# Kernel optimization log

Hardware: AMD Instinct MI355X
Metric: run time of the kernel (lower is better)

The kernel has to match this reference:

```python
import jax, jax.numpy as jnp
import numpy as np


def setup_inputs() -> dict:
    key = jax.random.key(0)
    k1, k2 = jax.random.split(key)
    x = jax.random.normal(k1, (4, 2048, 2048), dtype=jnp.float32)
    weight = jax.random.normal(k2, (8192, 2048), dtype=jnp.float32) * 0.02
    return {"x": x, "weight": weight, "bits": 8}


def reference(x, weight, bits):
    # ---- activation quantization (per-row int8-style) ----
    scale = jnp.clip(jnp.max(jnp.abs(x), axis=-1, keepdims=True), 1e-5)  # [..., 1]
    max_val = (1 << (bits - 1)) - 1  # 127 for 8 bits
    x_q = jnp.clip(jnp.round(x * (max_val / scale)), -max_val, max_val)

    # ---- ternary weight quantization (-1, 0, 1) ----
    w_scale = jnp.mean(jnp.abs(weight))
    w_q = jnp.where(weight > 0.5 * w_scale, 1.0, 0.0) + jnp.where(
        weight < -0.5 * w_scale, -1.0, 0.0
    )

    # ---- dequantized linear: (x_q @ (w_q * w_scale)^T) / x_scale ----
    out = jnp.einsum("bsi,oi->bso", x_q, w_q * w_scale) / scale

    # ---- squared ReLU ----
    return jnp.maximum(out, 0.0) ** 2
```

## Files before the change

kernel.cpp:

```cpp
#include <hip/hip_runtime.h>
#include <hip/hip_bf16.h>

typedef __attribute__((ext_vector_type(4))) int i32x4;
typedef __attribute__((ext_vector_type(16))) int i32x16;

#define M_DIM 8192
#define N_DIM 8192
#define K_DIM 2048
#define WCOUNT (N_DIM * K_DIM)

__global__ __launch_bounds__(256) void k_abs_partial(const float* __restrict__ w,
                                                     float* __restrict__ part) {
    int tid = blockIdx.x * 256 + threadIdx.x;
    const float4* w4 = (const float4*)w;
    float s = 0.0f;
    const int total4 = WCOUNT / 4;
    for (int i = tid; i < total4; i += 2048 * 256) {
        float4 v = w4[i];
        s += fabsf(v.x) + fabsf(v.y) + fabsf(v.z) + fabsf(v.w);
    }
    #pragma unroll
    for (int off = 1; off < 64; off <<= 1) s += __shfl_xor(s, off);
    __shared__ float red[4];
    if ((threadIdx.x & 63) == 0) red[threadIdx.x >> 6] = s;
    __syncthreads();
    if (threadIdx.x == 0)
        part[blockIdx.x] = (red[0] + red[1]) + (red[2] + red[3]);
}

__global__ __launch_bounds__(256) void k_abs_final(const float* __restrict__ part,
                                                   float* __restrict__ sum) {
    int t = threadIdx.x;
    float s = 0.0f;
    #pragma unroll
    for (int i = 0; i < 8; i++) s += part[t + i * 256];
    #pragma unroll
    for (int off = 1; off < 64; off <<= 1) s += __shfl_xor(s, off);
    __shared__ float red[4];
    if ((t & 63) == 0) red[t >> 6] = s;
    __syncthreads();
    if (t == 0) sum[0] = (red[0] + red[1]) + (red[2] + red[3]);
}

__global__ __launch_bounds__(256) void k_wquant(const float* __restrict__ w,
                                                const float* __restrict__ sum,
                                                unsigned int* __restrict__ wq) {
    const float thr = 0.5f * (sum[0] * (1.0f / 16777216.0f));
    int tid = blockIdx.x * 256 + threadIdx.x;
    const float4* w4 = (const float4*)w;
    const int total4 = WCOUNT / 4;
    for (int i = tid; i < total4; i += 2048 * 256) {
        float4 v = w4[i];
        union { signed char c[4]; unsigned int u; } q;
        q.c[0] = v.x > thr ? 1 : (v.x < -thr ? -1 : 0);
        q.c[1] = v.y > thr ? 1 : (v.y < -thr ? -1 : 0);
        q.c[2] = v.z > thr ? 1 : (v.z < -thr ? -1 : 0);
        q.c[3] = v.w > thr ? 1 : (v.w < -thr ? -1 : 0);
        wq[i] = q.u;
    }
}

__global__ __launch_bounds__(256) void k_xquant(const float* __restrict__ x,
                                                signed char* __restrict__ xq,
                                                float* __restrict__ scale) {
    const int row = blockIdx.x;
    const int t = threadIdx.x;
    const float4* xr = (const float4*)(x + (size_t)row * K_DIM);
    float4 a = xr[t * 2];
    float4 b = xr[t * 2 + 1];
    float m = fmaxf(fmaxf(fmaxf(fabsf(a.x), fabsf(a.y)), fmaxf(fabsf(a.z), fabsf(a.w))),
                    fmaxf(fmaxf(fabsf(b.x), fabsf(b.y)), fmaxf(fabsf(b.z), fabsf(b.w))));
    #pragma unroll
    for (int off = 1; off < 64; off <<= 1) m = fmaxf(m, __shfl_xor(m, off));
    __shared__ float red[4];
    if ((t & 63) == 0) red[t >> 6] = m;
    __syncthreads();
    m = fmaxf(fmaxf(red[0], red[1]), fmaxf(red[2], red[3]));
    const float sc = fmaxf(m, 1e-5f);
    if (t == 0) scale[row] = sc;
    const float r = 127.0f / sc;
    float q[8] = {a.x, a.y, a.z, a.w, b.x, b.y, b.z, b.w};
    union { signed char c[8]; uint2 v; } pk;
    #pragma unroll
    for (int j = 0; j < 8; j++) {
        float v = rintf(q[j] * r);
        v = fminf(fmaxf(v, -127.0f), 127.0f);
        pk.c[j] = (signed char)v;
    }
    *(uint2*)(xq + (size_t)row * K_DIM + t * 8) = pk.v;
}

__global__ __launch_bounds__(256) void k_coef(const float* __restrict__ sum,
                                              const float* __restrict__ scale,
                                              float* __restrict__ coef) {
    const int i = blockIdx.x * 256 + threadIdx.x;
    coef[i] = (sum[0] * (1.0f / 16777216.0f)) / scale[i];
}

#define GLDS16(g, l)                                                                   \
    __builtin_amdgcn_global_load_lds((const __attribute__((address_space(1))) void*)(g), \
                                     (__attribute__((address_space(3))) void*)(l), 16, 0, 0)

#define BAR __builtin_amdgcn_s_barrier()
#define VMCNT3 asm volatile("s_waitcnt vmcnt(3)" ::: "memory")
#define VMCNT0 asm volatile("s_waitcnt vmcnt(0)" ::: "memory")
#define ABUF(b) ((b) * 24576)
#define BBUF(b) ((b) * 24576 + 8192)

__global__ __launch_bounds__(512, 4) void k_gemm(const signed char* __restrict__ Aq,
                                                 const signed char* __restrict__ Bq,
                                                 const float* __restrict__ coef,
                                                 float* __restrict__ out) {
    __shared__ signed char lds[49152];

    const int t = threadIdx.x;
    const int lane = t & 63;
    const int wid = t >> 6;
    const int wm = wid >> 2;
    const int wn = wid & 3;
    const int l31 = lane & 31;
    const int kg = lane >> 5;

    const int bid = blockIdx.x;
    const int xcd = bid & 7;
    const int idx = bid >> 3;
    const int bcol = (idx >> 5) * 4 + (idx & 3);
    const int brow = xcd * 8 + ((idx >> 2) & 7);

    const int g4 = ((t & 3) ^ ((t >> 3) & 3)) << 4;
    const int arow_s = t >> 2;
    const int dstc = wid * 1024;

    const signed char* Abase = Aq + (size_t)(brow * 128) * K_DIM;
    const signed char* Bbase = Bq + (size_t)(bcol * 256) * K_DIM;

#define STG_K(buf, kt) do {                                                        \
        GLDS16(Abase + arow_s * K_DIM + (kt) * 64 + g4, lds + ABUF(buf) + dstc);   \
        GLDS16(Bbase + arow_s * K_DIM + (kt) * 64 + g4, lds + BBUF(buf) + dstc);   \
        GLDS16(Bbase + (128 + arow_s) * K_DIM + (kt) * 64 + g4,                    \
               lds + BBUF(buf) + 8192 + dstc); } while (0)

    const int rs = (l31 >> 1) & 3;
    const int ko0 = ((0 + kg) ^ rs) << 4;
    const int ko1 = ((2 + kg) ^ rs) << 4;
    const int aoff = (wm * 64 + l31) * 64;
    const int boff = 8192 + (wn * 64 + l31) * 64;

    i32x16 acc00 = (i32x16){0,0,0,0,0,0,0,0,0,0,0,0,0,0,0,0};
    i32x16 acc01 = acc00, acc10 = acc00, acc11 = acc00;

#define KTILE(buf) do {                                                            \
        const int ab = (buf) * 24576 + aoff;                                       \
        const int bb = (buf) * 24576 + boff;                                       \
        i32x4 a00 = *(const i32x4*)&lds[ab + ko0];                                 \
        i32x4 a10 = *(const i32x4*)&lds[ab + 2048 + ko0];                          \
        i32x4 b00 = *(const i32x4*)&lds[bb + ko0];                                 \
        i32x4 b10 = *(const i32x4*)&lds[bb + 2048 + ko0];                          \
        i32x4 a01 = *(const i32x4*)&lds[ab + ko1];                                 \
        i32x4 a11 = *(const i32x4*)&lds[ab + 2048 + ko1];                          \
        i32x4 b01 = *(const i32x4*)&lds[bb + ko1];                                 \
        i32x4 b11 = *(const i32x4*)&lds[bb + 2048 + ko1];                          \
        __builtin_amdgcn_s_setprio(1);                                             \
        acc00 = __builtin_amdgcn_mfma_i32_32x32x32_i8(a00, b00, acc00, 0, 0, 0);   \
        acc01 = __builtin_amdgcn_mfma_i32_32x32x32_i8(a00, b10, acc01, 0, 0, 0);   \
        acc10 = __builtin_amdgcn_mfma_i32_32x32x32_i8(a10, b00, acc10, 0, 0, 0);   \
        acc11 = __builtin_amdgcn_mfma_i32_32x32x32_i8(a10, b10, acc11, 0, 0, 0);   \
        acc00 = __builtin_amdgcn_mfma_i32_32x32x32_i8(a01, b01, acc00, 0, 0, 0);   \
        acc01 = __builtin_amdgcn_mfma_i32_32x32x32_i8(a01, b11, acc01, 0, 0, 0);   \
        acc10 = __builtin_amdgcn_mfma_i32_32x32x32_i8(a11, b01, acc10, 0, 0, 0);   \
        acc11 = __builtin_amdgcn_mfma_i32_32x32x32_i8(a11, b11, acc11, 0, 0, 0);   \
        __builtin_amdgcn_s_setprio(0); } while (0)

    STG_K(0, 0);
    STG_K(1, 1);
    VMCNT3;
    BAR;

    #pragma unroll 1
    for (int i = 0; i < 16; i++) {
        const int kt = 2 * i;
        KTILE(0);
        BAR;
        if (i < 15) { STG_K(0, kt + 2); VMCNT3; }
        else        { VMCNT0; }
        BAR;
        KTILE(1);
        if (i < 15) {
            BAR;
            STG_K(1, kt + 3); VMCNT3;
            BAR;
        }
    }

    const int rb = brow * 128 + wm * 64 + 4 * kg;
    const int cb = bcol * 256 + wn * 64 + l31;
    #pragma unroll
    for (int mt = 0; mt < 2; mt++) {
        const i32x16 ac0 = mt ? acc10 : acc00;
        const i32x16 ac1 = mt ? acc11 : acc01;
        #pragma unroll
        for (int r = 0; r < 16; r++) {
            const int grow = rb + mt * 32 + (r & 3) + 8 * (r >> 2);
            const float c = coef[grow];
            float v0 = (float)ac0[r] * c; v0 = fmaxf(v0, 0.0f);
            float v1 = (float)ac1[r] * c; v1 = fmaxf(v1, 0.0f);
            __builtin_nontemporal_store(v0 * v0, &out[(size_t)grow * N_DIM + cb]);
            __builtin_nontemporal_store(v1 * v1, &out[(size_t)grow * N_DIM + cb + 32]);
        }
    }
#undef STG_K
#undef KTILE
}

extern "C" void kernel_launch(void* const* d_in, const int* in_sizes, int n_in,
                              void* d_out, int out_size, void* d_ws, size_t ws_size,
                              hipStream_t stream) {
    const float* x = (const float*)d_in[0];
    const float* w = (const float*)d_in[1];
    float* out = (float*)d_out;

    char* ws = (char*)d_ws;
    float* sum   = (float*)ws;
    float* part  = (float*)(ws + 256);
    float* scale = (float*)(ws + 16384);
    float* coef  = (float*)(ws + 49152);
    signed char* xq = (signed char*)(ws + 131072);
    signed char* wq = (signed char*)(ws + 131072 + 16777216);

    k_abs_partial<<<2048, 256, 0, stream>>>(w, part);
    k_abs_final<<<1, 256, 0, stream>>>(part, sum);
    k_wquant<<<2048, 256, 0, stream>>>(w, sum, (unsigned int*)wq);
    k_xquant<<<M_DIM, 256, 0, stream>>>(x, xq, scale);
    k_coef<<<32, 256, 0, stream>>>(sum, scale, coef);
    k_gemm<<<dim3(2048), 512, 0, stream>>>(xq, wq, coef, out);
}
```

Baseline: 195.3 us.

## Pre-tile quantized operands into MFMA fragment layout and load B directly to registers

The quantize kernels now write int8 activations and ternary weights in a 32-row by 16-byte fragment-major tiled layout that matches the MFMA operand layout. The GEMM stages only A through LDS, shrinking LDS to 16KB. It loads B fragments straight from global memory into registers with a one-k-tile-ahead double buffer. This removes B LDS traffic and swizzle math and may raise occupancy, but makes B loads uncached per wave and more exposed to global latency.

```diff
diff --git a/kernel.cpp b/kernel.cpp
--- a/kernel.cpp
+++ b/kernel.cpp
@@ -8,6 +8,7 @@
 #define N_DIM 8192
 #define K_DIM 2048
 #define WCOUNT (N_DIM * K_DIM)
+
 
 __global__ __launch_bounds__(256) void k_abs_partial(const float* __restrict__ w,
                                                      float* __restrict__ part) {
@@ -44,24 +45,26 @@
 
 __global__ __launch_bounds__(256) void k_wquant(const float* __restrict__ w,
                                                 const float* __restrict__ sum,
-                                                unsigned int* __restrict__ wq) {
+                                                signed char* __restrict__ wqf) {
     const float thr = 0.5f * (sum[0] * (1.0f / 16777216.0f));
-    int tid = blockIdx.x * 256 + threadIdx.x;
-    const float4* w4 = (const float4*)w;
-    const int total4 = WCOUNT / 4;
-    for (int i = tid; i < total4; i += 2048 * 256) {
-        float4 v = w4[i];
-        union { signed char c[4]; unsigned int u; } q;
-        q.c[0] = v.x > thr ? 1 : (v.x < -thr ? -1 : 0);
-        q.c[1] = v.y > thr ? 1 : (v.y < -thr ? -1 : 0);
-        q.c[2] = v.z > thr ? 1 : (v.z < -thr ? -1 : 0);
-        q.c[3] = v.w > thr ? 1 : (v.w < -thr ? -1 : 0);
-        wq[i] = q.u;
-    }
+    const int g = blockIdx.x * 256 + threadIdx.x;
+    const int n = g >> 7;
+    const int kc = g & 127;
+    const float4* wr = (const float4*)(w + (size_t)n * K_DIM + kc * 16);
+    union { signed char c[16]; uint4 v; } pk;
+    #pragma unroll
+    for (int q = 0; q < 4; q++) {
+        float4 v = wr[q];
+        pk.c[q * 4 + 0] = v.x > thr ? 1 : (v.x < -thr ? -1 : 0);
+        pk.c[q * 4 + 1] = v.y > thr ? 1 : (v.y < -thr ? -1 : 0);
+        pk.c[q * 4 + 2] = v.z > thr ? 1 : (v.z < -thr ? -1 : 0);
+        pk.c[q * 4 + 3] = v.w > thr ? 1 : (v.w < -thr ? -1 : 0);
+    }
+    *(uint4*)(wqf + (size_t)(n >> 5) * 65536 + kc * 512 + (n & 31) * 16) = pk.v;
 }
 
 __global__ __launch_bounds__(256) void k_xquant(const float* __restrict__ x,
-                                                signed char* __restrict__ xq,
+                                                signed char* __restrict__ xqf,
                                                 float* __restrict__ scale) {
     const int row = blockIdx.x;
     const int t = threadIdx.x;
@@ -87,7 +90,8 @@
         v = fminf(fmaxf(v, -127.0f), 127.0f);
         pk.c[j] = (signed char)v;
     }
-    *(uint2*)(xq + (size_t)row * K_DIM + t * 8) = pk.v;
+    *(uint2*)(xqf + (size_t)(row >> 5) * 65536 + (t >> 1) * 512
+              + (row & 31) * 16 + (t & 1) * 8) = pk.v;
 }
 
 __global__ __launch_bounds__(256) void k_coef(const float* __restrict__ sum,
@@ -102,16 +106,14 @@
                                      (__attribute__((address_space(3))) void*)(l), 16, 0, 0)
 
 #define BAR __builtin_amdgcn_s_barrier()
-#define VMCNT3 asm volatile("s_waitcnt vmcnt(3)" ::: "memory")
-#define VMCNT0 asm volatile("s_waitcnt vmcnt(0)" ::: "memory")
-#define ABUF(b) ((b) * 24576)
-#define BBUF(b) ((b) * 24576 + 8192)
-
-__global__ __launch_bounds__(512, 4) void k_gemm(const signed char* __restrict__ Aq,
-                                                 const signed char* __restrict__ Bq,
+#define VMCNT5 asm volatile("s_waitcnt vmcnt(5)" ::: "memory")
+#define VMCNT4 asm volatile("s_waitcnt vmcnt(4)" ::: "memory")
+
+__global__ __launch_bounds__(512, 4) void k_gemm(const signed char* __restrict__ xqf,
+                                                 const signed char* __restrict__ wqf,
                                                  const float* __restrict__ coef,
                                                  float* __restrict__ out) {
-    __shared__ signed char lds[49152];
+    __shared__ signed char lds[16384];
 
     const int t = threadIdx.x;
     const int lane = t & 63;
@@ -127,70 +129,71 @@
     const int bcol = (idx >> 5) * 4 + (idx & 3);
     const int brow = xcd * 8 + ((idx >> 2) & 7);
 
-    const int g4 = ((t & 3) ^ ((t >> 3) & 3)) << 4;
-    const int arow_s = t >> 2;
-    const int dstc = wid * 1024;
-
-    const signed char* Abase = Aq + (size_t)(brow * 128) * K_DIM;
-    const signed char* Bbase = Bq + (size_t)(bcol * 256) * K_DIM;
-
-#define STG_K(buf, kt) do {                                                        \
-        GLDS16(Abase + arow_s * K_DIM + (kt) * 64 + g4, lds + ABUF(buf) + dstc);   \
-        GLDS16(Bbase + arow_s * K_DIM + (kt) * 64 + g4, lds + BBUF(buf) + dstc);   \
-        GLDS16(Bbase + (128 + arow_s) * K_DIM + (kt) * 64 + g4,                    \
-               lds + BBUF(buf) + 8192 + dstc); } while (0)
-
-    const int rs = (l31 >> 1) & 3;
-    const int ko0 = ((0 + kg) ^ rs) << 4;
-    const int ko1 = ((2 + kg) ^ rs) << 4;
-    const int aoff = (wm * 64 + l31) * 64;
-    const int boff = 8192 + (wn * 64 + l31) * 64;
+    const signed char* aSrc = xqf + (size_t)(brow * 4 + (t >> 7)) * 65536
+                              + ((t >> 5) & 3) * 512 + (t & 31) * 16;
+    const int aDst = wid * 1024;
+
+    const signed char* bSrc = wqf + (size_t)(bcol * 8 + wn * 2) * 65536 + lane * 16;
+
+    const int aRd = wm * 4096 + lane * 16;
 
     i32x16 acc00 = (i32x16){0,0,0,0,0,0,0,0,0,0,0,0,0,0,0,0};
     i32x16 acc01 = acc00, acc10 = acc00, acc11 = acc00;
 
-#define KTILE(buf) do {                                                            \
-        const int ab = (buf) * 24576 + aoff;                                       \
-        const int bb = (buf) * 24576 + boff;                                       \
-        i32x4 a00 = *(const i32x4*)&lds[ab + ko0];                                 \
-        i32x4 a10 = *(const i32x4*)&lds[ab + 2048 + ko0];                          \
-        i32x4 b00 = *(const i32x4*)&lds[bb + ko0];                                 \
-        i32x4 b10 = *(const i32x4*)&lds[bb + 2048 + ko0];                          \
-        i32x4 a01 = *(const i32x4*)&lds[ab + ko1];                                 \
-        i32x4 a11 = *(const i32x4*)&lds[ab + 2048 + ko1];                          \
-        i32x4 b01 = *(const i32x4*)&lds[bb + ko1];                                 \
-        i32x4 b11 = *(const i32x4*)&lds[bb + 2048 + ko1];                          \
+#define STG_A(buf, kt) GLDS16(aSrc + (size_t)(kt) * 2048, lds + (buf) * 8192 + aDst)
+#define LOADB(B0, B1, B2, B3, kt) do {                                             \
+        B0 = *(const i32x4*)(bSrc + (size_t)(kt) * 2048);                          \
+        B1 = *(const i32x4*)(bSrc + (size_t)(kt) * 2048 + 65536);                  \
+        B2 = *(const i32x4*)(bSrc + (size_t)(kt) * 2048 + 1024);                   \
+        B3 = *(const i32x4*)(bSrc + (size_t)(kt) * 2048 + 66560); } while (0)
+#define HALF(buf, B0, B1, B2, B3) do {                                             \
+        i32x4 a0 = *(const i32x4*)&lds[(buf) * 8192 + aRd];                        \
+        i32x4 a1 = *(const i32x4*)&lds[(buf) * 8192 + aRd + 2048];                 \
         __builtin_amdgcn_s_setprio(1);                                             \
-        acc00 = __builtin_amdgcn_mfma_i32_32x32x32_i8(a00, b00, acc00, 0, 0, 0);   \
-        acc01 = __builtin_amdgcn_mfma_i32_32x32x32_i8(a00, b10, acc01, 0, 0, 0);   \
-        acc10 = __builtin_amdgcn_mfma_i32_32x32x32_i8(a10, b00, acc10, 0, 0, 0);   \
-        acc11 = __builtin_amdgcn_mfma_i32_32x32x32_i8(a10, b10, acc11, 0, 0, 0);   \
-        acc00 = __builtin_amdgcn_mfma_i32_32x32x32_i8(a01, b01, acc00, 0, 0, 0);   \
-        acc01 = __builtin_amdgcn_mfma_i32_32x32x32_i8(a01, b11, acc01, 0, 0, 0);   \
-        acc10 = __builtin_amdgcn_mfma_i32_32x32x32_i8(a11, b01, acc10, 0, 0, 0);   \
-        acc11 = __builtin_amdgcn_mfma_i32_32x32x32_i8(a11, b11, acc11, 0, 0, 0);   \
+        acc00 = __builtin_amdgcn_mfma_i32_32x32x32_i8(a0, B0, acc00, 0, 0, 0);     \
+        acc01 = __builtin_amdgcn_mfma_i32_32x32x32_i8(a0, B1, acc01, 0, 0, 0);     \
+        acc10 = __builtin_amdgcn_mfma_i32_32x32x32_i8(a1, B0, acc10, 0, 0, 0);     \
+        acc11 = __builtin_amdgcn_mfma_i32_32x32x32_i8(a1, B1, acc11, 0, 0, 0);     \
+        __builtin_amdgcn_s_setprio(0);                                             \
+        a0 = *(const i32x4*)&lds[(buf) * 8192 + aRd + 1024];                       \
+        a1 = *(const i32x4*)&lds[(buf) * 8192 + aRd + 3072];                       \
+        __builtin_amdgcn_s_setprio(1);                                             \
+        acc00 = __builtin_amdgcn_mfma_i32_32x32x32_i8(a0, B2, acc00, 0, 0, 0);     \
+        acc01 = __builtin_amdgcn_mfma_i32_32x32x32_i8(a0, B3, acc01, 0, 0, 0);     \
+        acc10 = __builtin_amdgcn_mfma_i32_32x32x32_i8(a1, B2, acc10, 0, 0, 0);     \
+        acc11 = __builtin_amdgcn_mfma_i32_32x32x32_i8(a1, B3, acc11, 0, 0, 0);     \
         __builtin_amdgcn_s_setprio(0); } while (0)
 
-    STG_K(0, 0);
-    STG_K(1, 1);
-    VMCNT3;
+    i32x4 BA0, BA1, BA2, BA3, BB0, BB1, BB2, BB3;
+
+    STG_A(0, 0);
+    STG_A(1, 1);
+    LOADB(BA0, BA1, BA2, BA3, 0);
+    VMCNT5;
     BAR;
 
     #pragma unroll 1
-    for (int i = 0; i < 16; i++) {
-        const int kt = 2 * i;
-        KTILE(0);
-        BAR;
-        if (i < 15) { STG_K(0, kt + 2); VMCNT3; }
-        else        { VMCNT0; }
-        BAR;
-        KTILE(1);
-        if (i < 15) {
-            BAR;
-            STG_K(1, kt + 3); VMCNT3;
-            BAR;
-        }
-    }
+    for (int j = 0; j < 15; j++) {
+        const int kt = 2 * j;
+        LOADB(BB0, BB1, BB2, BB3, kt + 1);
+        HALF(0, BA0, BA1, BA2, BA3);
+        BAR;
+        STG_A(0, kt + 2);
+        VMCNT5;
+        BAR;
+        LOADB(BA0, BA1, BA2, BA3, kt + 2);
+        HALF(1, BB0, BB1, BB2, BB3);
+        BAR;
+        STG_A(1, kt + 3);
+        VMCNT5;
+        BAR;
+    }
+    LOADB(BB0, BB1, BB2, BB3, 31);
+    HALF(0, BA0, BA1, BA2, BA3);
+    BAR;
+    VMCNT4;
+    BAR;
+    HALF(1, BB0, BB1, BB2, BB3);
 
     const int rb = brow * 128 + wm * 64 + 4 * kg;
     const int cb = bcol * 256 + wn * 64 + l31;
@@ -208,8 +211,9 @@
             __builtin_nontemporal_store(v1 * v1, &out[(size_t)grow * N_DIM + cb + 32]);
         }
     }
-#undef STG_K
-#undef KTILE
+#undef STG_A
+#undef LOADB
+#undef HALF
 }
 
 extern "C" void kernel_launch(void* const* d_in, const int* in_sizes, int n_in,
@@ -224,13 +228,13 @@
     float* part  = (float*)(ws + 256);
     float* scale = (float*)(ws + 16384);
     float* coef  = (float*)(ws + 49152);
-    signed char* xq = (signed char*)(ws + 131072);
-    signed char* wq = (signed char*)(ws + 131072 + 16777216);
+    signed char* xqf = (signed char*)(ws + 131072);
+    signed char* wqf = (signed char*)(ws + 131072 + 16777216);
 
     k_abs_partial<<<2048, 256, 0, stream>>>(w, part);
     k_abs_final<<<1, 256, 0, stream>>>(part, sum);
-    k_wquant<<<2048, 256, 0, stream>>>(w, sum, (unsigned int*)wq);
-    k_xquant<<<M_DIM, 256, 0, stream>>>(x, xq, scale);
+    k_wquant<<<4096, 256, 0, stream>>>(w, sum, wqf);
+    k_xquant<<<M_DIM, 256, 0, stream>>>(x, xqf, scale);
     k_coef<<<32, 256, 0, stream>>>(sum, scale, coef);
-    k_gemm<<<dim3(2048), 512, 0, stream>>>(xq, wq, coef, out);
-}
+    k_gemm<<<dim3(2048), 512, 0, stream>>>(xqf, wqf, coef, out);
+}
```

Result: slower. 203.9 us (+4.4%).
